# Kernel tuning notes

Hardware: AMD Instinct MI355X
Metric: run time of the kernel (lower is better)

## Reference

```python
import jax, jax.numpy as jnp
import numpy as np

SEQ_LEN, BATCH, INPUT, HID, LAYERS, TARGET_LEN = 120, 2048, 6, 64, 4, 120


def _cell(x_t, h, c, Wih, Whh, b):
    # torch LSTM gate order: input, forget, cell(g), output
    gates = x_t @ Wih.T + h @ Whh.T + b  # [B, 4H]
    i, f, g, o = jnp.split(gates, 4, axis=-1)
    c_new = jax.nn.sigmoid(f) * c + jax.nn.sigmoid(i) * jnp.tanh(g)
    h_new = jax.nn.sigmoid(o) * jnp.tanh(c_new)
    return h_new, c_new


def _stack_step(h, c, x_t, Wih0, Wih, Whh, b):
    # one time step through all stacked layers; h, c: [L, B, H]
    hs, cs = [], []
    inp = x_t
    L = Whh.shape[0]
    for l in range(L):
        W = Wih0 if l == 0 else Wih[l - 1]
        hn, cn = _cell(inp, h[l], c[l], W, Whh[l], b[l])
        hs.append(hn)
        cs.append(cn)
        inp = hn
    return jnp.stack(hs), jnp.stack(cs), inp


def setup_inputs() -> dict:
    key = jax.random.key(0)
    ks = jax.random.split(key, 11)
    s = 1.0 / np.sqrt(HID)  # torch LSTM uniform init scale
    u = lambda k, shp: jax.random.uniform(k, shp, jnp.float32, -s, s)
    return {
        "x": jax.random.normal(ks[0], (SEQ_LEN, BATCH, INPUT), jnp.float32),
        "enc_Wih0": u(ks[1], (4 * HID, INPUT)),
        "enc_Wih": u(ks[2], (LAYERS - 1, 4 * HID, HID)),
        "enc_Whh": u(ks[3], (LAYERS, 4 * HID, HID)),
        "enc_b": u(ks[4], (LAYERS, 4 * HID)),
        "dec_Wih0": u(ks[5], (4 * HID, INPUT)),
        "dec_Wih": u(ks[6], (LAYERS - 1, 4 * HID, HID)),
        "dec_Whh": u(ks[7], (LAYERS, 4 * HID, HID)),
        "dec_b": u(ks[8], (LAYERS, 4 * HID)),
        "lin_W": u(ks[9], (INPUT, HID)),
        "lin_b": u(ks[10], (INPUT,)),
        "target_len": TARGET_LEN,
    }


def reference(x, enc_Wih0, enc_Wih, enc_Whh, enc_b,
              dec_Wih0, dec_Wih, dec_Whh, dec_b, lin_W, lin_b, target_len):
    L, B, H = enc_Whh.shape[0], x.shape[1], enc_Whh.shape[-1]
    h0 = jnp.zeros((L, B, H), x.dtype)

    # ---- encoder: stacked LSTM over the input sequence (zero init state) ----
    def enc_step(carry, x_t):
        h, c = carry
        h, c, _ = _stack_step(h, c, x_t, enc_Wih0, enc_Wih, enc_Whh, enc_b)
        return (h, c), None

    (h, c), _ = jax.lax.scan(enc_step, (h0, h0), x)

    # ---- decoder: recursive one-step decode for target_len steps ----
    def dec_step(carry, _):
        h, c, inp = carry
        h, c, top = _stack_step(h, c, inp, dec_Wih0, dec_Wih, dec_Whh, dec_b)
        out = top @ lin_W.T + lin_b  # [B, INPUT]
        return (h, c, out), out

    last_in = x[-1]  # decoder seeded with last observed frame
    _, outputs = jax.lax.scan(dec_step, (h, c, last_in), None, length=target_len)
    return outputs  # [target_len, B, INPUT]
```

## Files before the change

### kernel.cpp

```cpp
#include <hip/hip_runtime.h>


#define S_LEN 120
#define BATCH 2048
#define NIN   6
#define H     64
#define NL    4
#define TLEN  120

#define HPAD 72

#define FRAGS_HALF 60
#define PACK_H8    (2 * FRAGS_HALF * 4 * 64)
#define PROJ_H8    (2 * 64)
#define NPACK      ((PACK_H8 + PROJ_H8) * 8)
#define EPACK_EL   (256 * 64 * 8)
#define NTOT       (NPACK + EPACK_EL)

#define WS_HOFF (768 * 1024)
#define WS_COFF (WS_HOFF + 1024 * 1024)

#define PERM(kk) ((((kk) & 3) << 4) | ((kk) >> 2))
#define PI(c)    ((((c) & 15) << 2) | ((c) >> 4))

typedef _Float16 h8    __attribute__((ext_vector_type(8)));
typedef _Float16 hh2   __attribute__((ext_vector_type(2)));
typedef float    f32x4 __attribute__((ext_vector_type(4)));

__device__ __forceinline__ void bar_lgkm() {
  asm volatile("s_waitcnt lgkmcnt(0)\n\ts_barrier" ::: "memory");
}

__global__ void prep_weights(const float* __restrict__ eWih0,
                             const float* __restrict__ eWih,
                             const float* __restrict__ eWhh,
                             const float* __restrict__ dWih0,
                             const float* __restrict__ dWih,
                             const float* __restrict__ dWhh,
                             const float* __restrict__ linW,
                             _Float16* __restrict__ wq) {
  int idx = blockIdx.x * blockDim.x + threadIdx.x;
  if (idx >= NTOT) return;

  if (idx >= NPACK) {
    int p    = idx - NPACK;
    int j    = p & 7;
    int lane = (p >> 3) & 63;
    int fe   = p >> 9;
    int kt   = fe & 3, nt = (fe >> 2) & 15, l = fe >> 6;
    int g    = nt * 16 + (lane & 15);
    int koff = ((lane >> 4) << 3) + j;
    float v = 0.0f;
    if (l == 0) {
      if (kt == 0)      v = (koff < NIN) ? eWih0[g * NIN + koff] : 0.0f;
      else if (kt == 1) v = 0.0f;
      else { int kk = (kt - 2) * 32 + koff; v = eWhh[g * H + PERM(kk)]; }
    } else {
      if (kt < 2) { int kk = kt * 32 + koff;
                    v = eWih[((l - 1) * 256 + g) * H + PERM(kk)]; }
      else        { int kk = (kt - 2) * 32 + koff;
                    v = eWhh[(l * 256 + g) * H + PERM(kk)]; }
    }
    wq[idx] = (_Float16)v;
    return;
  }

  if (idx >= PACK_H8 * 8) {
    int p    = idx - PACK_H8 * 8;
    int j    = p & 7;
    int lane = (p >> 3) & 63;
    int fr   = p >> 9;
    int m    = lane & 15;
    int k    = fr * 32 + ((lane >> 4) << 3) + j;
    wq[idx] = (_Float16)((m < NIN) ? linW[m * H + k] : 0.0f);
    return;
  }

  const int j    = idx & 7;
  const int lane = (idx >> 3) & 63;
  const int wv   = (idx >> 9) & 3;
  const int fh   = idx >> 11;
  const int f    = fh % FRAGS_HALF;
  const int half = fh / FRAGS_HALF;
  const float* Wi0 = half ? dWih0 : eWih0;
  const float* Wi  = half ? dWih  : eWih;
  const float* Wh  = half ? dWhh  : eWhh;
  int l, q, kt;
  if (f < 12) { l = 0; q = f / 3; kt = f % 3; }
  else        { int ff = f - 12; l = 1 + ff / 16; ff %= 16; q = ff / 4; kt = ff % 4; }
  const int g    = q * 64 + wv * 16 + (lane & 15);
  const int k_in = ((lane >> 4) << 3) + j;
  float v;
  if (l == 0) {
    if (kt == 0) v = (k_in < NIN) ? Wi0[g * NIN + k_in] : 0.0f;
    else         v = Wh[g * H + (kt - 1) * 32 + k_in];
  } else {
    if (kt < 2) v = Wi[((l - 1) * 256 + g) * H + kt * 32 + k_in];
    else        v = Wh[(l * 256 + g) * H + (kt - 2) * 32 + k_in];
  }
  wq[idx] = (_Float16)v;
}

__device__ __forceinline__ float rcpf(float x) { return __builtin_amdgcn_rcpf(x); }
__device__ __forceinline__ f32x4 mf(h8 a, h8 b, f32x4 c) {
  return __builtin_amdgcn_mfma_f32_16x16x32_f16(a, b, c, 0, 0, 0);
}
#define SPLAT(v) ((f32x4){(v), (v), (v), (v)})

__device__ __forceinline__ float ew_one(float gi, float gf, float gg, float go,
                                        float& c) {
  gg = fminf(fmaxf(gg, -20.0f), 20.0f);
  float eni = __expf(-gi);
  float e2g = __expf(2.0f * gg);
  float enf = __expf(-gf);
  float eno = __expf(-go);
  c = c * rcpf(1.0f + enf) + (e2g - 1.0f) * rcpf((1.0f + eni) * (e2g + 1.0f));
  float cc = fminf(fmaxf(c, -20.0f), 20.0f);
  float e2c = __expf(2.0f * cc);
  return (e2c - 1.0f) * rcpf((1.0f + eno) * (e2c + 1.0f));
}

__device__ __forceinline__ void cell_ew(f32x4 g0, f32x4 g1, f32x4 g2, f32x4 g3,
                                        f32x4& c, _Float16* outbuf,
                                        int quad, int r16, int lw) {
  #pragma unroll
  for (int r = 0; r < 4; r++) {
    float cv = c[r];
    float hv = ew_one(g0[r], g1[r], g2[r], g3[r], cv);
    c[r] = cv;
    outbuf[(quad * 4 + r) * HPAD + lw * 16 + r16] = (_Float16)hv;
  }
}
__device__ __forceinline__ void fireH(const h8 (&w)[16], h8 ai0, h8 ai1,
                                      const f32x4 (&ac)[4], f32x4& c,
                                      _Float16* outbuf, int quad, int r16, int lw) {
  f32x4 g0 = mf(ai1, w[1],  mf(ai0, w[0],  ac[0]));
  f32x4 g1 = mf(ai1, w[5],  mf(ai0, w[4],  ac[1]));
  f32x4 g2 = mf(ai1, w[9],  mf(ai0, w[8],  ac[2]));
  f32x4 g3 = mf(ai1, w[13], mf(ai0, w[12], ac[3]));
  cell_ew(g0, g1, g2, g3, c, outbuf, quad, r16, lw);
}
__device__ __forceinline__ void precH(const h8 (&w)[16], h8 ar0, h8 ar1,
                                      f32x4 b, f32x4 (&ac)[4]) {
  ac[0] = mf(ar1, w[3],  mf(ar0, w[2],  SPLAT(b[0])));
  ac[1] = mf(ar1, w[7],  mf(ar0, w[6],  SPLAT(b[1])));
  ac[2] = mf(ar1, w[11], mf(ar0, w[10], SPLAT(b[2])));
  ac[3] = mf(ar1, w[15], mf(ar0, w[14], SPLAT(b[3])));
}
__device__ __forceinline__ void fire0(const h8 (&w)[12], h8 ax,
                                      const f32x4 (&ac)[4], f32x4& c,
                                      _Float16* outbuf, int quad, int r16, int lw) {
  f32x4 g0 = mf(ax, w[0], ac[0]);
  f32x4 g1 = mf(ax, w[3], ac[1]);
  f32x4 g2 = mf(ax, w[6], ac[2]);
  f32x4 g3 = mf(ax, w[9], ac[3]);
  cell_ew(g0, g1, g2, g3, c, outbuf, quad, r16, lw);
}
__device__ __forceinline__ void prec0(const h8 (&w)[12], h8 ar0, h8 ar1,
                                      f32x4 b, f32x4 (&ac)[4]) {
  ac[0] = mf(ar1, w[2],  mf(ar0, w[1],  SPLAT(b[0])));
  ac[1] = mf(ar1, w[5],  mf(ar0, w[4],  SPLAT(b[1])));
  ac[2] = mf(ar1, w[8],  mf(ar0, w[7],  SPLAT(b[2])));
  ac[3] = mf(ar1, w[11], mf(ar0, w[10], SPLAT(b[3])));
}
__device__ __forceinline__ void readA(const _Float16* buf, int r16, int quad,
                                      h8& a0, h8& a1) {
  a0 = *(const h8*)(buf + r16 * HPAD + quad * 8);
  a1 = *(const h8*)(buf + r16 * HPAD + 32 + quad * 8);
}

__global__ void __launch_bounds__(512, 2)
lstm_enc(const float* __restrict__ X,
         const float* __restrict__ encb,
         const h8* __restrict__ WQ,
         _Float16* __restrict__ hG,
         float* __restrict__ cG) {
  __shared__ _Float16 Hb[NL][2][16][HPAD];
  __shared__ _Float16 Xb[2][16][HPAD];

  const int tid  = threadIdx.x;
  const int wv   = tid >> 6;
  const int lane = tid & 63;
  const int quad = lane >> 4;
  const int r16  = lane & 15;
  const int grp  = wv >> 2;
  const int lw   = wv & 3;
  const int bbase = blockIdx.x * 16;

  {
    float* p = (float*)&Hb[0][0][0][0];
    for (int i = tid; i < 4608; i += 512) p[i] = 0.0f;
    float* px = (float*)&Xb[0][0][0];
    for (int i = tid; i < 1152; i += 512) if (i < 1152) px[i] = 0.0f;
  }
  if (tid < 16 * NIN) {
    int m = tid / NIN, ii = tid - m * NIN;
    Xb[0][m][ii] = (_Float16)X[((size_t)0 * BATCH + bbase + m) * NIN + ii];
  }

  h8 we[8][4];
  #pragma unroll
  for (int q = 0; q < 4; q++)
    #pragma unroll
    for (int cc = 0; cc < 2; cc++)
      #pragma unroll
      for (int kt = 0; kt < 4; kt++)
        we[q * 2 + cc][kt] =
            WQ[(PACK_H8 + PROJ_H8) +
               ((lw * 64 + (q * 4 + 2 * grp + cc) * 4 + kt) * 64 + lane)];
  float ben[8];
  #pragma unroll
  for (int q = 0; q < 4; q++)
    #pragma unroll
    for (int cc = 0; cc < 2; cc++)
      ben[q * 2 + cc] = encb[lw * 256 + q * 64 + (2 * grp + cc) * 16 + r16];

  f32x4 ce[2];
  ce[0] = SPLAT(0.f); ce[1] = SPLAT(0.f);

  const bool pfLane = (wv == 0) && (lane < 48);
  const int  pe0 = lane * 2, pe1 = pe0 + 1;
  const int  pm0 = pe0 / NIN, pc0 = pe0 % NIN;
  const int  pm1 = pe1 / NIN, pc1 = pe1 % NIN;
  float pf0 = 0.f, pf1 = 0.f;
  if (pfLane) {
    const float* xs = X + ((size_t)1 * BATCH + bbase) * NIN;
    pf0 = xs[pe0]; pf1 = xs[pe1];
  }

  __syncthreads();

  #pragma unroll 1
  for (int i = 0; i < S_LEN + NL - 1; i++) {
    const int p = i & 1;
    const bool active = (i >= lw) && (i - lw < S_LEN);
    if (active) {
      const _Float16* inb = (lw == 0) ? &Xb[p][0][0] : &Hb[lw - 1][p ^ 1][0][0];
      const _Float16* rcb = &Hb[lw][p ^ 1][0][0];
      h8 ai0 = *(const h8*)(inb + r16 * HPAD + quad * 8);
      h8 ai1 = {};
      if (lw) ai1 = *(const h8*)(inb + r16 * HPAD + 32 + quad * 8);
      h8 ar0 = *(const h8*)(rcb + r16 * HPAD + quad * 8);
      h8 ar1 = *(const h8*)(rcb + r16 * HPAD + 32 + quad * 8);

      float nf0 = 0.f, nf1 = 0.f;
      if (pfLane && (i + 2 < S_LEN)) {
        const float* xs = X + ((size_t)(i + 2) * BATCH + bbase) * NIN;
        nf0 = xs[pe0]; nf1 = xs[pe1];
      }

      f32x4 a[8];
      #pragma unroll
      for (int j = 0; j < 8; j++) {
        f32x4 t = SPLAT(ben[j]);
        t = mf(ai0, we[j][0], t);
        if (lw) t = mf(ai1, we[j][1], t);
        t = mf(ar0, we[j][2], t);
        t = mf(ar1, we[j][3], t);
        a[j] = t;
      }

      _Float16* wb = &Hb[lw][p][0][0];
      #pragma unroll
      for (int r = 0; r < 4; r++) {
        hh2 hv;
        #pragma unroll
        for (int cc = 0; cc < 2; cc++) {
          float cv = ce[cc][r];
          hv[cc] = (_Float16)ew_one(a[cc][r], a[2 + cc][r],
                                    a[4 + cc][r], a[6 + cc][r], cv);
          ce[cc][r] = cv;
        }
        *(hh2*)(wb + (quad * 4 + r) * HPAD + 4 * r16 + 2 * grp) = hv;
      }

      if (pfLane && (i + 1 < S_LEN)) {
        Xb[p ^ 1][pm0][pc0] = (_Float16)pf0;
        Xb[p ^ 1][pm1][pc1] = (_Float16)pf1;
      }
      pf0 = nf0; pf1 = nf1;
    }
    bar_lgkm();
  }

  #pragma unroll
  for (int cc = 0; cc < 2; cc++)
    #pragma unroll
    for (int r = 0; r < 4; r++)
      cG[((size_t)lw * BATCH + bbase + quad * 4 + r) * H +
         (2 * grp + cc) * 16 + r16] = ce[cc][r];

  #pragma unroll
  for (int u = 0; u < 8; u++) {
    int i2 = tid + u * 512;
    int c = i2 & 63, m = (i2 >> 6) & 15, l = (i2 >> 10) & 3;
    hG[((size_t)l * BATCH + bbase + m) * H + c] =
        Hb[l][(l + 1) & 1][m][PI(c)];
  }
}

__global__ void __launch_bounds__(256, 1)
lstm_dec(const float* __restrict__ X,
         const float* __restrict__ decb,
         const float* __restrict__ linb,
         const h8* __restrict__ WQ,
         const _Float16* __restrict__ hG,
         const float* __restrict__ cG,
         float* __restrict__ out) {
  __shared__ _Float16 Hb[NL][2][16][HPAD];

  const int tid   = threadIdx.x;
  const int lw    = tid >> 6;
  const int lane  = tid & 63;
  const int quad  = lane >> 4;
  const int r16   = lane & 15;
  const int bbase = blockIdx.x * 16;

  #pragma unroll
  for (int u = 0; u < 16; u++) {
    int i2 = tid + u * 256;
    int l = i2 >> 10, m = (i2 >> 6) & 15, c = i2 & 63;
    Hb[l][1][m][c] = hG[((size_t)l * BATCH + bbase + m) * H + c];
  }

  f32x4 cs0, cs1, cs2, cs3;
  #pragma unroll
  for (int r = 0; r < 4; r++) {
    cs0[r] = cG[((size_t)0 * BATCH + bbase + quad * 4 + r) * H + lw * 16 + r16];
    cs1[r] = cG[((size_t)1 * BATCH + bbase + quad * 4 + r) * H + lw * 16 + r16];
    cs2[r] = cG[((size_t)2 * BATCH + bbase + quad * 4 + r) * H + lw * 16 + r16];
    cs3[r] = cG[((size_t)3 * BATCH + bbase + quad * 4 + r) * H + lw * 16 + r16];
  }

  h8 w0[12], w1[16], w2[16], w3[16];
  #pragma unroll
  for (int f = 0; f < 12; f++) w0[f] = WQ[((FRAGS_HALF + f)      * 4 + lw) * 64 + lane];
  #pragma unroll
  for (int f = 0; f < 16; f++) w1[f] = WQ[((FRAGS_HALF + 12 + f) * 4 + lw) * 64 + lane];
  #pragma unroll
  for (int f = 0; f < 16; f++) w2[f] = WQ[((FRAGS_HALF + 28 + f) * 4 + lw) * 64 + lane];
  #pragma unroll
  for (int f = 0; f < 16; f++) w3[f] = WQ[((FRAGS_HALF + 44 + f) * 4 + lw) * 64 + lane];

  f32x4 b0, b1, b2, b3;
  #pragma unroll
  for (int q = 0; q < 4; q++) {
    b0[q] = decb[0 * 256 + q * 64 + lw * 16 + r16];
    b1[q] = decb[1 * 256 + q * 64 + lw * 16 + r16];
    b2[q] = decb[2 * 256 + q * 64 + lw * 16 + r16];
    b3[q] = decb[3 * 256 + q * 64 + lw * 16 + r16];
  }

  h8 lwA0 = WQ[PACK_H8 + lane];
  h8 lwA1 = WQ[PACK_H8 + 64 + lane];
  f32x4 lbq;
  #pragma unroll
  for (int r = 0; r < 4; r++)
    lbq[r] = (quad * 4 + r < NIN) ? linb[quad * 4 + r] : 0.0f;

  h8 xseed = {};
  if (quad == 0) {
    const float* xs = X + ((size_t)(S_LEN - 1) * BATCH + bbase + r16) * NIN;
    #pragma unroll
    for (int j = 0; j < 6; j++) xseed[j] = (_Float16)xs[j];
  }

  __syncthreads();

  f32x4 ac0[4], ac1[4], ac2[4], ac3[4];
  {
    h8 s0, s1;
    readA(&Hb[0][1][0][0], r16, quad, s0, s1); prec0(w0, s0, s1, b0, ac0);
    readA(&Hb[1][1][0][0], r16, quad, s0, s1); precH(w1, s0, s1, b1, ac1);
    readA(&Hb[2][1][0][0], r16, quad, s0, s1); precH(w2, s0, s1, b2, ac2);
  }

  #pragma unroll 1
  for (int t = 0; t < TLEN; t++) {
    const int cur = t & 1, prv = cur ^ 1;
    {
      h8 ar0, ar1;
      readA(&Hb[3][prv][0][0], r16, quad, ar0, ar1);
      h8 ax;
      if (t == 0) {
        ax = xseed;
      } else {
        f32x4 ap = lbq;
        ap = mf(lwA0, ar0, ap);
        ap = mf(lwA1, ar1, ap);
        if (lw == 0) {
          #pragma unroll
          for (int r = 0; r < 4; r++) {
            const int fm = quad * 4 + r;
            if (fm < NIN)
              out[((size_t)(t - 1) * BATCH + bbase + r16) * NIN + fm] = ap[r];
          }
        }
        float x0 = __shfl(ap[0], r16);
        float x1 = __shfl(ap[1], r16);
        float x2 = __shfl(ap[2], r16);
        float x3 = __shfl(ap[3], r16);
        float x4 = __shfl(ap[0], 16 + r16);
        float x5 = __shfl(ap[1], 16 + r16);
        h8 xa = {};
        xa[0] = (_Float16)x0; xa[1] = (_Float16)x1; xa[2] = (_Float16)x2;
        xa[3] = (_Float16)x3; xa[4] = (_Float16)x4; xa[5] = (_Float16)x5;
        h8 zz = {};
        ax = (quad == 0) ? xa : zz;
      }
      precH(w3, ar0, ar1, b3, ac3);
      fire0(w0, ax, ac0, cs0, &Hb[0][cur][0][0], quad, r16, lw);
      bar_lgkm();
    }
    {
      h8 ai0, ai1;
      readA(&Hb[0][cur][0][0], r16, quad, ai0, ai1);
      fireH(w1, ai0, ai1, ac1, cs1, &Hb[1][cur][0][0], quad, r16, lw);
      prec0(w0, ai0, ai1, b0, ac0);
      bar_lgkm();
    }
    {
      h8 ai0, ai1;
      readA(&Hb[1][cur][0][0], r16, quad, ai0, ai1);
      fireH(w2, ai0, ai1, ac2, cs2, &Hb[2][cur][0][0], quad, r16, lw);
      precH(w1, ai0, ai1, b1, ac1);
      bar_lgkm();
    }
    {
      h8 ai0, ai1;
      readA(&Hb[2][cur][0][0], r16, quad, ai0, ai1);
      fireH(w3, ai0, ai1, ac3, cs3, &Hb[3][cur][0][0], quad, r16, lw);
      precH(w2, ai0, ai1, b2, ac2);
      bar_lgkm();
    }
  }

  if (lw == 0) {
    h8 ar0, ar1;
    readA(&Hb[3][1][0][0], r16, quad, ar0, ar1);
    f32x4 ap = lbq;
    ap = mf(lwA0, ar0, ap);
    ap = mf(lwA1, ar1, ap);
    #pragma unroll
    for (int r = 0; r < 4; r++) {
      const int fm = quad * 4 + r;
      if (fm < NIN)
        out[((size_t)(TLEN - 1) * BATCH + bbase + r16) * NIN + fm] = ap[r];
    }
  }
}

extern "C" void kernel_launch(void* const* d_in, const int* in_sizes, int n_in,
                              void* d_out, int out_size, void* d_ws, size_t ws_size,
                              hipStream_t stream) {
  const float* X     = (const float*)d_in[0];
  const float* eWih0 = (const float*)d_in[1];
  const float* eWih  = (const float*)d_in[2];
  const float* eWhh  = (const float*)d_in[3];
  const float* eb    = (const float*)d_in[4];
  const float* dWih0 = (const float*)d_in[5];
  const float* dWih  = (const float*)d_in[6];
  const float* dWhh  = (const float*)d_in[7];
  const float* db    = (const float*)d_in[8];
  const float* lW    = (const float*)d_in[9];
  const float* lb    = (const float*)d_in[10];

  _Float16* wq = (_Float16*)d_ws;
  _Float16* hG = (_Float16*)((char*)d_ws + WS_HOFF);
  float*    cG = (float*)((char*)d_ws + WS_COFF);

  prep_weights<<<(NTOT + 255) / 256, 256, 0, stream>>>(
      eWih0, eWih, eWhh, dWih0, dWih, dWhh, lW, wq);

  lstm_enc<<<BATCH / 16, 512, 0, stream>>>(
      X, eb, (const h8*)wq, hG, cG);

  lstm_dec<<<BATCH / 16, 256, 0, stream>>>(
      X, db, lb, (const h8*)wq, hG, cG, (float*)d_out);
}
```

Measured before the change: 568.7 us.

## Split encoder gate columns across 16 waves per block instead of 8

Measured after the change: 628.9 us. 1.11x slower.

```diff
diff --git a/kernel.cpp b/kernel.cpp
--- a/kernel.cpp
+++ b/kernel.cpp
@@ -169,7 +169,7 @@
   a1 = *(const h8*)(buf + r16 * HPAD + 32 + quad * 8);
 }
 
-__global__ void __launch_bounds__(512, 2)
+__global__ void __launch_bounds__(1024, 4)
 lstm_enc(const float* __restrict__ X,
          const float* __restrict__ encb,
          const h8* __restrict__ WQ,
@@ -183,49 +183,41 @@
   const int lane = tid & 63;
   const int quad = lane >> 4;
   const int r16  = lane & 15;
-  const int grp  = wv >> 2;
+  const int sl   = wv >> 2;
   const int lw   = wv & 3;
   const int bbase = blockIdx.x * 16;
 
   {
     float* p = (float*)&Hb[0][0][0][0];
-    for (int i = tid; i < 4608; i += 512) p[i] = 0.0f;
+    for (int i = tid; i < 4608; i += 1024) p[i] = 0.0f;
     float* px = (float*)&Xb[0][0][0];
-    for (int i = tid; i < 1152; i += 512) if (i < 1152) px[i] = 0.0f;
+    for (int i = tid; i < 1152; i += 1024) px[i] = 0.0f;
   }
   if (tid < 16 * NIN) {
     int m = tid / NIN, ii = tid - m * NIN;
     Xb[0][m][ii] = (_Float16)X[((size_t)0 * BATCH + bbase + m) * NIN + ii];
   }
 
-  h8 we[8][4];
+  h8 we[4][4];
   #pragma unroll
   for (int q = 0; q < 4; q++)
     #pragma unroll
-    for (int cc = 0; cc < 2; cc++)
-      #pragma unroll
-      for (int kt = 0; kt < 4; kt++)
-        we[q * 2 + cc][kt] =
-            WQ[(PACK_H8 + PROJ_H8) +
-               ((lw * 64 + (q * 4 + 2 * grp + cc) * 4 + kt) * 64 + lane)];
-  float ben[8];
+    for (int kt = 0; kt < 4; kt++)
+      we[q][kt] =
+          WQ[(PACK_H8 + PROJ_H8) +
+             ((lw * 64 + (q * 4 + sl) * 4 + kt) * 64 + lane)];
+  f32x4 ben;
   #pragma unroll
   for (int q = 0; q < 4; q++)
-    #pragma unroll
-    for (int cc = 0; cc < 2; cc++)
-      ben[q * 2 + cc] = encb[lw * 256 + q * 64 + (2 * grp + cc) * 16 + r16];
-
-  f32x4 ce[2];
-  ce[0] = SPLAT(0.f); ce[1] = SPLAT(0.f);
+    ben[q] = encb[lw * 256 + q * 64 + sl * 16 + r16];
+
+  f32x4 ce = SPLAT(0.f);
 
   const bool pfLane = (wv == 0) && (lane < 48);
-  const int  pe0 = lane * 2, pe1 = pe0 + 1;
-  const int  pm0 = pe0 / NIN, pc0 = pe0 % NIN;
-  const int  pm1 = pe1 / NIN, pc1 = pe1 % NIN;
   float pf0 = 0.f, pf1 = 0.f;
   if (pfLane) {
     const float* xs = X + ((size_t)1 * BATCH + bbase) * NIN;
-    pf0 = xs[pe0]; pf1 = xs[pe1];
+    pf0 = xs[lane * 2]; pf1 = xs[lane * 2 + 1];
   }
 
   __syncthreads();
@@ -246,37 +238,33 @@
       float nf0 = 0.f, nf1 = 0.f;
       if (pfLane && (i + 2 < S_LEN)) {
         const float* xs = X + ((size_t)(i + 2) * BATCH + bbase) * NIN;
-        nf0 = xs[pe0]; nf1 = xs[pe1];
+        nf0 = xs[lane * 2]; nf1 = xs[lane * 2 + 1];
       }
 
-      f32x4 a[8];
+      f32x4 a[4];
       #pragma unroll
-      for (int j = 0; j < 8; j++) {
-        f32x4 t = SPLAT(ben[j]);
-        t = mf(ai0, we[j][0], t);
-        if (lw) t = mf(ai1, we[j][1], t);
-        t = mf(ar0, we[j][2], t);
-        t = mf(ar1, we[j][3], t);
-        a[j] = t;
+      for (int q = 0; q < 4; q++) {
+        f32x4 t = SPLAT(ben[q]);
+        t = mf(ai0, we[q][0], t);
+        if (lw) t = mf(ai1, we[q][1], t);
+        t = mf(ar0, we[q][2], t);
+        t = mf(ar1, we[q][3], t);
+        a[q] = t;
       }
 
       _Float16* wb = &Hb[lw][p][0][0];
       #pragma unroll
       for (int r = 0; r < 4; r++) {
-        hh2 hv;
-        #pragma unroll
-        for (int cc = 0; cc < 2; cc++) {
-          float cv = ce[cc][r];
-          hv[cc] = (_Float16)ew_one(a[cc][r], a[2 + cc][r],
-                                    a[4 + cc][r], a[6 + cc][r], cv);
-          ce[cc][r] = cv;
-        }
-        *(hh2*)(wb + (quad * 4 + r) * HPAD + 4 * r16 + 2 * grp) = hv;
+        float cv = ce[r];
+        float hv = ew_one(a[0][r], a[1][r], a[2][r], a[3][r], cv);
+        ce[r] = cv;
+        wb[(quad * 4 + r) * HPAD + 4 * r16 + sl] = (_Float16)hv;
       }
 
       if (pfLane && (i + 1 < S_LEN)) {
-        Xb[p ^ 1][pm0][pc0] = (_Float16)pf0;
-        Xb[p ^ 1][pm1][pc1] = (_Float16)pf1;
+        const int pe0 = lane * 2, pe1 = pe0 + 1;
+        Xb[p ^ 1][pe0 / NIN][pe0 % NIN] = (_Float16)pf0;
+        Xb[p ^ 1][pe1 / NIN][pe1 % NIN] = (_Float16)pf1;
       }
       pf0 = nf0; pf1 = nf1;
     }
@@ -284,15 +272,12 @@
   }
 
   #pragma unroll
-  for (int cc = 0; cc < 2; cc++)
-    #pragma unroll
-    for (int r = 0; r < 4; r++)
-      cG[((size_t)lw * BATCH + bbase + quad * 4 + r) * H +
-         (2 * grp + cc) * 16 + r16] = ce[cc][r];
-
-  #pragma unroll
-  for (int u = 0; u < 8; u++) {
-    int i2 = tid + u * 512;
+  for (int r = 0; r < 4; r++)
+    cG[((size_t)lw * BATCH + bbase + quad * 4 + r) * H + sl * 16 + r16] = ce[r];
+
+  #pragma unroll
+  for (int u = 0; u < 4; u++) {
+    int i2 = tid + u * 1024;
     int c = i2 & 63, m = (i2 >> 6) & 15, l = (i2 >> 10) & 3;
     hG[((size_t)l * BATCH + bbase + m) * H + c] =
         Hb[l][(l + 1) & 1][m][PI(c)];
@@ -472,7 +457,7 @@
   prep_weights<<<(NTOT + 255) / 256, 256, 0, stream>>>(
       eWih0, eWih, eWhh, dWih0, dWih, dWhh, lW, wq);
 
-  lstm_enc<<<BATCH / 16, 512, 0, stream>>>(
+  lstm_enc<<<BATCH / 16, 1024, 0, stream>>>(
       X, eb, (const h8*)wq, hG, cG);
 
   lstm_dec<<<BATCH / 16, 256, 0, stream>>>(
```

## Split decoder into producer and consumer waves exchanging recurrent partial gates via LDS

Applied to the files above, without the earlier changes.

New measurement: 604.7 us. 6.3% more time.

```diff
diff --git a/kernel.cpp b/kernel.cpp
--- a/kernel.cpp
+++ b/kernel.cpp
@@ -122,46 +122,39 @@
 
 __device__ __forceinline__ void cell_ew(f32x4 g0, f32x4 g1, f32x4 g2, f32x4 g3,
                                         f32x4& c, _Float16* outbuf,
-                                        int quad, int r16, int lw) {
+                                        int quad, int r16, int sl) {
   #pragma unroll
   for (int r = 0; r < 4; r++) {
     float cv = c[r];
     float hv = ew_one(g0[r], g1[r], g2[r], g3[r], cv);
     c[r] = cv;
-    outbuf[(quad * 4 + r) * HPAD + lw * 16 + r16] = (_Float16)hv;
-  }
-}
-__device__ __forceinline__ void fireH(const h8 (&w)[16], h8 ai0, h8 ai1,
-                                      const f32x4 (&ac)[4], f32x4& c,
-                                      _Float16* outbuf, int quad, int r16, int lw) {
-  f32x4 g0 = mf(ai1, w[1],  mf(ai0, w[0],  ac[0]));
-  f32x4 g1 = mf(ai1, w[5],  mf(ai0, w[4],  ac[1]));
-  f32x4 g2 = mf(ai1, w[9],  mf(ai0, w[8],  ac[2]));
-  f32x4 g3 = mf(ai1, w[13], mf(ai0, w[12], ac[3]));
-  cell_ew(g0, g1, g2, g3, c, outbuf, quad, r16, lw);
-}
-__device__ __forceinline__ void precH(const h8 (&w)[16], h8 ar0, h8 ar1,
+    outbuf[(quad * 4 + r) * HPAD + sl * 16 + r16] = (_Float16)hv;
+  }
+}
+
+__device__ __forceinline__ void precc(const h8 (&w)[8], h8 ar0, h8 ar1,
                                       f32x4 b, f32x4 (&ac)[4]) {
-  ac[0] = mf(ar1, w[3],  mf(ar0, w[2],  SPLAT(b[0])));
-  ac[1] = mf(ar1, w[7],  mf(ar0, w[6],  SPLAT(b[1])));
-  ac[2] = mf(ar1, w[11], mf(ar0, w[10], SPLAT(b[2])));
-  ac[3] = mf(ar1, w[15], mf(ar0, w[14], SPLAT(b[3])));
-}
-__device__ __forceinline__ void fire0(const h8 (&w)[12], h8 ax,
-                                      const f32x4 (&ac)[4], f32x4& c,
-                                      _Float16* outbuf, int quad, int r16, int lw) {
+  #pragma unroll
+  for (int q = 0; q < 4; q++)
+    ac[q] = mf(ar1, w[q * 2 + 1], mf(ar0, w[q * 2], SPLAT(b[q])));
+}
+__device__ __forceinline__ void fireHc(const h8 (&w)[8], h8 ai0, h8 ai1,
+                                       const f32x4 (&ac)[4], f32x4& c,
+                                       _Float16* outbuf, int quad, int r16, int sl) {
+  f32x4 g0 = mf(ai1, w[1], mf(ai0, w[0], ac[0]));
+  f32x4 g1 = mf(ai1, w[3], mf(ai0, w[2], ac[1]));
+  f32x4 g2 = mf(ai1, w[5], mf(ai0, w[4], ac[2]));
+  f32x4 g3 = mf(ai1, w[7], mf(ai0, w[6], ac[3]));
+  cell_ew(g0, g1, g2, g3, c, outbuf, quad, r16, sl);
+}
+__device__ __forceinline__ void fire0c(const h8 (&w)[4], h8 ax,
+                                       const f32x4 (&ac)[4], f32x4& c,
+                                       _Float16* outbuf, int quad, int r16, int sl) {
   f32x4 g0 = mf(ax, w[0], ac[0]);
-  f32x4 g1 = mf(ax, w[3], ac[1]);
-  f32x4 g2 = mf(ax, w[6], ac[2]);
-  f32x4 g3 = mf(ax, w[9], ac[3]);
-  cell_ew(g0, g1, g2, g3, c, outbuf, quad, r16, lw);
-}
-__device__ __forceinline__ void prec0(const h8 (&w)[12], h8 ar0, h8 ar1,
-                                      f32x4 b, f32x4 (&ac)[4]) {
-  ac[0] = mf(ar1, w[2],  mf(ar0, w[1],  SPLAT(b[0])));
-  ac[1] = mf(ar1, w[5],  mf(ar0, w[4],  SPLAT(b[1])));
-  ac[2] = mf(ar1, w[8],  mf(ar0, w[7],  SPLAT(b[2])));
-  ac[3] = mf(ar1, w[11], mf(ar0, w[10], SPLAT(b[3])));
+  f32x4 g1 = mf(ax, w[1], ac[1]);
+  f32x4 g2 = mf(ax, w[2], ac[2]);
+  f32x4 g3 = mf(ax, w[3], ac[3]);
+  cell_ew(g0, g1, g2, g3, c, outbuf, quad, r16, sl);
 }
 __device__ __forceinline__ void readA(const _Float16* buf, int r16, int quad,
                                       h8& a0, h8& a1) {
@@ -299,7 +292,7 @@
   }
 }
 
-__global__ void __launch_bounds__(256, 1)
+__global__ void __launch_bounds__(512, 2)
 lstm_dec(const float* __restrict__ X,
          const float* __restrict__ decb,
          const float* __restrict__ linb,
@@ -308,144 +301,216 @@
          const float* __restrict__ cG,
          float* __restrict__ out) {
   __shared__ _Float16 Hb[NL][2][16][HPAD];
+  __shared__ f32x4 ACs[NL][4][64][4];
 
   const int tid   = threadIdx.x;
-  const int lw    = tid >> 6;
+  const int wv    = tid >> 6;
+  const int sl    = wv & 3;
+  const int roleP = wv >> 2;
   const int lane  = tid & 63;
   const int quad  = lane >> 4;
   const int r16   = lane & 15;
   const int bbase = blockIdx.x * 16;
 
   #pragma unroll
-  for (int u = 0; u < 16; u++) {
-    int i2 = tid + u * 256;
+  for (int u = 0; u < 8; u++) {
+    int i2 = tid + u * 512;
     int l = i2 >> 10, m = (i2 >> 6) & 15, c = i2 & 63;
     Hb[l][1][m][c] = hG[((size_t)l * BATCH + bbase + m) * H + c];
   }
-
-  f32x4 cs0, cs1, cs2, cs3;
-  #pragma unroll
-  for (int r = 0; r < 4; r++) {
-    cs0[r] = cG[((size_t)0 * BATCH + bbase + quad * 4 + r) * H + lw * 16 + r16];
-    cs1[r] = cG[((size_t)1 * BATCH + bbase + quad * 4 + r) * H + lw * 16 + r16];
-    cs2[r] = cG[((size_t)2 * BATCH + bbase + quad * 4 + r) * H + lw * 16 + r16];
-    cs3[r] = cG[((size_t)3 * BATCH + bbase + quad * 4 + r) * H + lw * 16 + r16];
-  }
-
-  h8 w0[12], w1[16], w2[16], w3[16];
-  #pragma unroll
-  for (int f = 0; f < 12; f++) w0[f] = WQ[((FRAGS_HALF + f)      * 4 + lw) * 64 + lane];
-  #pragma unroll
-  for (int f = 0; f < 16; f++) w1[f] = WQ[((FRAGS_HALF + 12 + f) * 4 + lw) * 64 + lane];
-  #pragma unroll
-  for (int f = 0; f < 16; f++) w2[f] = WQ[((FRAGS_HALF + 28 + f) * 4 + lw) * 64 + lane];
-  #pragma unroll
-  for (int f = 0; f < 16; f++) w3[f] = WQ[((FRAGS_HALF + 44 + f) * 4 + lw) * 64 + lane];
-
-  f32x4 b0, b1, b2, b3;
-  #pragma unroll
-  for (int q = 0; q < 4; q++) {
-    b0[q] = decb[0 * 256 + q * 64 + lw * 16 + r16];
-    b1[q] = decb[1 * 256 + q * 64 + lw * 16 + r16];
-    b2[q] = decb[2 * 256 + q * 64 + lw * 16 + r16];
-    b3[q] = decb[3 * 256 + q * 64 + lw * 16 + r16];
-  }
-
-  h8 lwA0 = WQ[PACK_H8 + lane];
-  h8 lwA1 = WQ[PACK_H8 + 64 + lane];
-  f32x4 lbq;
-  #pragma unroll
-  for (int r = 0; r < 4; r++)
-    lbq[r] = (quad * 4 + r < NIN) ? linb[quad * 4 + r] : 0.0f;
-
-  h8 xseed = {};
-  if (quad == 0) {
-    const float* xs = X + ((size_t)(S_LEN - 1) * BATCH + bbase + r16) * NIN;
-    #pragma unroll
-    for (int j = 0; j < 6; j++) xseed[j] = (_Float16)xs[j];
-  }
-
   __syncthreads();
 
-  f32x4 ac0[4], ac1[4], ac2[4], ac3[4];
-  {
-    h8 s0, s1;
-    readA(&Hb[0][1][0][0], r16, quad, s0, s1); prec0(w0, s0, s1, b0, ac0);
-    readA(&Hb[1][1][0][0], r16, quad, s0, s1); precH(w1, s0, s1, b1, ac1);
-    readA(&Hb[2][1][0][0], r16, quad, s0, s1); precH(w2, s0, s1, b2, ac2);
-  }
-
-  #pragma unroll 1
-  for (int t = 0; t < TLEN; t++) {
-    const int cur = t & 1, prv = cur ^ 1;
+  if (roleP) {
+    h8 wp0[8], wpH[3][8];
+    #pragma unroll
+    for (int e = 0; e < 8; e++) {
+      int q = e >> 1, k = e & 1;
+      wp0[e] = WQ[((FRAGS_HALF + q * 3 + 1 + k) * 4 + sl) * 64 + lane];
+    }
+    #pragma unroll
+    for (int l = 0; l < 3; l++)
+      #pragma unroll
+      for (int e = 0; e < 8; e++) {
+        int q = e >> 1, k = e & 1;
+        wpH[l][e] = WQ[((FRAGS_HALF + 12 + l * 16 + q * 4 + 2 + k) * 4 + sl) * 64 + lane];
+      }
+    f32x4 b0, b1, b2, b3;
+    #pragma unroll
+    for (int q = 0; q < 4; q++) {
+      b0[q] = decb[0 * 256 + q * 64 + sl * 16 + r16];
+      b1[q] = decb[1 * 256 + q * 64 + sl * 16 + r16];
+      b2[q] = decb[2 * 256 + q * 64 + sl * 16 + r16];
+      b3[q] = decb[3 * 256 + q * 64 + sl * 16 + r16];
+    }
+
     {
+      h8 s0, s1;
+      f32x4 a[4];
+      readA(&Hb[0][1][0][0], r16, quad, s0, s1);
+      precc(wp0, s0, s1, b0, a);
+      #pragma unroll
+      for (int j = 0; j < 4; j++) ACs[0][sl][lane][j] = a[j];
+      readA(&Hb[1][1][0][0], r16, quad, s0, s1);
+      precc(wpH[0], s0, s1, b1, a);
+      #pragma unroll
+      for (int j = 0; j < 4; j++) ACs[1][sl][lane][j] = a[j];
+      readA(&Hb[2][1][0][0], r16, quad, s0, s1);
+      precc(wpH[1], s0, s1, b2, a);
+      #pragma unroll
+      for (int j = 0; j < 4; j++) ACs[2][sl][lane][j] = a[j];
+    }
+    bar_lgkm();
+
+    #pragma unroll 1
+    for (int t = 0; t < TLEN; t++) {
+      const int cur = t & 1, prv = cur ^ 1;
+      {
+        h8 a0, a1; readA(&Hb[3][prv][0][0], r16, quad, a0, a1);
+        f32x4 a[4]; precc(wpH[2], a0, a1, b3, a);
+        #pragma unroll
+        for (int j = 0; j < 4; j++) ACs[3][sl][lane][j] = a[j];
+        bar_lgkm();
+      }
+      {
+        h8 a0, a1; readA(&Hb[0][cur][0][0], r16, quad, a0, a1);
+        f32x4 a[4]; precc(wp0, a0, a1, b0, a);
+        #pragma unroll
+        for (int j = 0; j < 4; j++) ACs[0][sl][lane][j] = a[j];
+        bar_lgkm();
+      }
+      {
+        h8 a0, a1; readA(&Hb[1][cur][0][0], r16, quad, a0, a1);
+        f32x4 a[4]; precc(wpH[0], a0, a1, b1, a);
+        #pragma unroll
+        for (int j = 0; j < 4; j++) ACs[1][sl][lane][j] = a[j];
+        bar_lgkm();
+      }
+      {
+        h8 a0, a1; readA(&Hb[2][cur][0][0], r16, quad, a0, a1);
+        f32x4 a[4]; precc(wpH[1], a0, a1, b2, a);
+        #pragma unroll
+        for (int j = 0; j < 4; j++) ACs[2][sl][lane][j] = a[j];
+        bar_lgkm();
+      }
+    }
+  } else {
+    h8 wf0[4], wfH[3][8];
+    #pragma unroll
+    for (int q = 0; q < 4; q++)
+      wf0[q] = WQ[((FRAGS_HALF + q * 3) * 4 + sl) * 64 + lane];
+    #pragma unroll
+    for (int l = 0; l < 3; l++)
+      #pragma unroll
+      for (int e = 0; e < 8; e++) {
+        int q = e >> 1, k = e & 1;
+        wfH[l][e] = WQ[((FRAGS_HALF + 12 + l * 16 + q * 4 + k) * 4 + sl) * 64 + lane];
+      }
+
+    f32x4 cs0, cs1, cs2, cs3;
+    #pragma unroll
+    for (int r = 0; r < 4; r++) {
+      cs0[r] = cG[((size_t)0 * BATCH + bbase + quad * 4 + r) * H + sl * 16 + r16];
+      cs1[r] = cG[((size_t)1 * BATCH + bbase + quad * 4 + r) * H + sl * 16 + r16];
+      cs2[r] = cG[((size_t)2 * BATCH + bbase + quad * 4 + r) * H + sl * 16 + r16];
+      cs3[r] = cG[((size_t)3 * BATCH + bbase + quad * 4 + r) * H + sl * 16 + r16];
+    }
+
+    h8 lwA0 = WQ[PACK_H8 + lane];
+    h8 lwA1 = WQ[PACK_H8 + 64 + lane];
+    f32x4 lbq;
+    #pragma unroll
+    for (int r = 0; r < 4; r++)
+      lbq[r] = (quad * 4 + r < NIN) ? linb[quad * 4 + r] : 0.0f;
+
+    h8 xseed = {};
+    if (quad == 0) {
+      const float* xs = X + ((size_t)(S_LEN - 1) * BATCH + bbase + r16) * NIN;
+      #pragma unroll
+      for (int j = 0; j < 6; j++) xseed[j] = (_Float16)xs[j];
+    }
+
+    bar_lgkm();
+
+    #pragma unroll 1
+    for (int t = 0; t < TLEN; t++) {
+      const int cur = t & 1, prv = cur ^ 1;
+      {
+        h8 ar0, ar1;
+        readA(&Hb[3][prv][0][0], r16, quad, ar0, ar1);
+        h8 ax;
+        if (t == 0) {
+          ax = xseed;
+        } else {
+          f32x4 ap = lbq;
+          ap = mf(lwA0, ar0, ap);
+          ap = mf(lwA1, ar1, ap);
+          if (sl == 0) {
+            #pragma unroll
+            for (int r = 0; r < 4; r++) {
+              const int fm = quad * 4 + r;
+              if (fm < NIN)
+                out[((size_t)(t - 1) * BATCH + bbase + r16) * NIN + fm] = ap[r];
+            }
+          }
+          float x0 = __shfl(ap[0], r16);
+          float x1 = __shfl(ap[1], r16);
+          float x2 = __shfl(ap[2], r16);
+          float x3 = __shfl(ap[3], r16);
+          float x4 = __shfl(ap[0], 16 + r16);
+          float x5 = __shfl(ap[1], 16 + r16);
+          h8 xa = {};
+          xa[0] = (_Float16)x0; xa[1] = (_Float16)x1; xa[2] = (_Float16)x2;
+          xa[3] = (_Float16)x3; xa[4] = (_Float16)x4; xa[5] = (_Float16)x5;
+          h8 zz = {};
+          ax = (quad == 0) ? xa : zz;
+        }
+        f32x4 ac[4];
+        #pragma unroll
+        for (int j = 0; j < 4; j++) ac[j] = ACs[0][sl][lane][j];
+        fire0c(wf0, ax, ac, cs0, &Hb[0][cur][0][0], quad, r16, sl);
+        bar_lgkm();
+      }
+      {
+        h8 ai0, ai1;
+        readA(&Hb[0][cur][0][0], r16, quad, ai0, ai1);
+        f32x4 ac[4];
+        #pragma unroll
+        for (int j = 0; j < 4; j++) ac[j] = ACs[1][sl][lane][j];
+        fireHc(wfH[0], ai0, ai1, ac, cs1, &Hb[1][cur][0][0], quad, r16, sl);
+        bar_lgkm();
+      }
+      {
+        h8 ai0, ai1;
+        readA(&Hb[1][cur][0][0], r16, quad, ai0, ai1);
+        f32x4 ac[4];
+        #pragma unroll
+        for (int j = 0; j < 4; j++) ac[j] = ACs[2][sl][lane][j];
+        fireHc(wfH[1], ai0, ai1, ac, cs2, &Hb[2][cur][0][0], quad, r16, sl);
+        bar_lgkm();
+      }
+      {
+        h8 ai0, ai1;
+        readA(&Hb[2][cur][0][0], r16, quad, ai0, ai1);
+        f32x4 ac[4];
+        #pragma unroll
+        for (int j = 0; j < 4; j++) ac[j] = ACs[3][sl][lane][j];
+        fireHc(wfH[2], ai0, ai1, ac, cs3, &Hb[3][cur][0][0], quad, r16, sl);
+        bar_lgkm();
+      }
+    }
+
+    if (sl == 0) {
       h8 ar0, ar1;
-      readA(&Hb[3][prv][0][0], r16, quad, ar0, ar1);
-      h8 ax;
-      if (t == 0) {
-        ax = xseed;
-      } else {
-        f32x4 ap = lbq;
-        ap = mf(lwA0, ar0, ap);
-        ap = mf(lwA1, ar1, ap);
-        if (lw == 0) {
-          #pragma unroll
-          for (int r = 0; r < 4; r++) {
-            const int fm = quad * 4 + r;
-            if (fm < NIN)
-              out[((size_t)(t - 1) * BATCH + bbase + r16) * NIN + fm] = ap[r];
-          }
-        }
-        float x0 = __shfl(ap[0], r16);
-        float x1 = __shfl(ap[1], r16);
-        float x2 = __shfl(ap[2], r16);
-        float x3 = __shfl(ap[3], r16);
-        float x4 = __shfl(ap[0], 16 + r16);
-        float x5 = __shfl(ap[1], 16 + r16);
-        h8 xa = {};
-        xa[0] = (_Float16)x0; xa[1] = (_Float16)x1; xa[2] = (_Float16)x2;
-        xa[3] = (_Float16)x3; xa[4] = (_Float16)x4; xa[5] = (_Float16)x5;
-        h8 zz = {};
-        ax = (quad == 0) ? xa : zz;
-      }
-      precH(w3, ar0, ar1, b3, ac3);
-      fire0(w0, ax, ac0, cs0, &Hb[0][cur][0][0], quad, r16, lw);
-      bar_lgkm();
-    }
-    {
-      h8 ai0, ai1;
-      readA(&Hb[0][cur][0][0], r16, quad, ai0, ai1);
-      fireH(w1, ai0, ai1, ac1, cs1, &Hb[1][cur][0][0], quad, r16, lw);
-      prec0(w0, ai0, ai1, b0, ac0);
-      bar_lgkm();
-    }
-    {
-      h8 ai0, ai1;
-      readA(&Hb[1][cur][0][0], r16, quad, ai0, ai1);
-      fireH(w2, ai0, ai1, ac2, cs2, &Hb[2][cur][0][0], quad, r16, lw);
-      precH(w1, ai0, ai1, b1, ac1);
-      bar_lgkm();
-    }
-    {
-      h8 ai0, ai1;
-      readA(&Hb[2][cur][0][0], r16, quad, ai0, ai1);
-      fireH(w3, ai0, ai1, ac3, cs3, &Hb[3][cur][0][0], quad, r16, lw);
-      precH(w2, ai0, ai1, b2, ac2);
-      bar_lgkm();
-    }
-  }
-
-  if (lw == 0) {
-    h8 ar0, ar1;
-    readA(&Hb[3][1][0][0], r16, quad, ar0, ar1);
-    f32x4 ap = lbq;
-    ap = mf(lwA0, ar0, ap);
-    ap = mf(lwA1, ar1, ap);
-    #pragma unroll
-    for (int r = 0; r < 4; r++) {
-      const int fm = quad * 4 + r;
-      if (fm < NIN)
-        out[((size_t)(TLEN - 1) * BATCH + bbase + r16) * NIN + fm] = ap[r];
+      readA(&Hb[3][1][0][0], r16, quad, ar0, ar1);
+      f32x4 ap = lbq;
+      ap = mf(lwA0, ar0, ap);
+      ap = mf(lwA1, ar1, ap);
+      #pragma unroll
+      for (int r = 0; r < 4; r++) {
+        const int fm = quad * 4 + r;
+        if (fm < NIN)
+          out[((size_t)(TLEN - 1) * BATCH + bbase + r16) * NIN + fm] = ap[r];
+      }
     }
   }
 }
@@ -475,6 +540,6 @@
   lstm_enc<<<BATCH / 16, 512, 0, stream>>>(
       X, eb, (const h8*)wq, hG, cG);
 
-  lstm_dec<<<BATCH / 16, 256, 0, stream>>>(
+  lstm_dec<<<BATCH / 16, 512, 0, stream>>>(
       X, db, lb, (const h8*)wq, hG, cG, (float*)d_out);
 }
```
